# Performance work log

Hardware: AMD Instinct MI355X
Metric: run time of the kernel (lower is better)

Reference implementation:

```python
import jax, jax.numpy as jnp
import numpy as np

N_NODES = 10000
N_EDGES = 640000
D_IN = 128
D_OUT = 128


def setup_inputs() -> dict:
    key = jax.random.key(0)
    k1, k2, k3, k4 = jax.random.split(key, 4)
    x = jax.random.normal(k1, (N_NODES, D_IN), dtype=jnp.float32)
    # PyG GCNConv weight: [dim_out, dim_in] (glorot)
    W = jax.random.normal(k2, (D_OUT, D_IN), dtype=jnp.float32) * (1.0 / np.sqrt(D_IN))
    b = jnp.zeros((D_OUT,), dtype=jnp.float32)
    edge_weight = jax.random.uniform(k3, (N_EDGES,), dtype=jnp.float32)
    edge_index = jax.random.randint(k4, (2, N_EDGES), 0, N_NODES, dtype=jnp.int32)
    return {"x": x, "W": W, "b": b, "edge_weight": edge_weight, "edge_index": edge_index}


def reference(x, W, b, edge_weight, edge_index):
    N = x.shape[0]
    # --- add self loops (fill weight = 1.0), PyG default ---
    loops = jnp.arange(N, dtype=edge_index.dtype)
    src = jnp.concatenate([edge_index[0], loops])
    dst = jnp.concatenate([edge_index[1], loops])
    ew = jnp.concatenate([edge_weight, jnp.ones((N,), dtype=edge_weight.dtype)])
    # --- symmetric GCN normalization: deg from target index ---
    deg = jax.ops.segment_sum(ew, dst, num_segments=N)
    dinv = jnp.where(deg > 0, jax.lax.rsqrt(deg), 0.0)
    norm = dinv[src] * ew * dinv[dst]  # [E+N]
    # --- linear transform then gather-scale-scatter aggregation ---
    h = x @ W.T  # [N, D_OUT]
    msgs = h[src] * norm[:, None]  # [E+N, D_OUT]
    out = jax.ops.segment_sum(msgs, dst, num_segments=N)
    return out + b
```

## Files before the change

### kernel.cpp

```cpp
#include <hip/hip_runtime.h>

#define N_NODES 10000
#define N_EDGES 640000
#define D 128
#define CAP 128

typedef unsigned long long ull;
typedef unsigned short u16;
typedef unsigned int u32;

#define CHUNKS 256
#define EPC 2500
#define GEMM_NPB 32
#define GEMM_BLOCKS ((N_NODES + GEMM_NPB - 1) / GEMM_NPB)
#define SMEM_BYTES 40000
#define EWFX 262144.0f
#define EWM  0x1ffffffu

__device__ __forceinline__ u16 f2bf(float f) {
    unsigned u = __float_as_uint(f);
    unsigned r = (u + 0x7fffu + ((u >> 16) & 1u)) >> 16;
    return (u16)r;
}


__global__ void __launch_bounds__(256, 4) k_hist_fill_gemm(
    const int* __restrict__ src, const int* __restrict__ dst,
    const float* __restrict__ ew, u32* __restrict__ gpacked,
    const float* __restrict__ x, const float* __restrict__ W,
    u16* __restrict__ h_bf, ull* __restrict__ csr)
{
    extern __shared__ char smem[];
    const int t = threadIdx.x;

    if (blockIdx.x < CHUNKS) {
        u32* hist = (u32*)smem;
        ull* h8 = (ull*)smem;
        for (int i = t; i < N_NODES / 2; i += 256) h8[i] = 0;
        __syncthreads();

        const int e0 = blockIdx.x * EPC;
        u32 dlr[10];
        float ewr[10];
        #pragma unroll
        for (int i = 0; i < 10; ++i) {
            int idx = i * 256 + t;
            dlr[i] = 0xffffffffu;
            if (idx < EPC) {
                int e = e0 + idx;
                int d = dst[e];
                float w = ew[e];
                ewr[i] = w;
                u32 add = (1u << 25) | (u32)(w * EWFX);
                u32 old = atomicAdd(&hist[d], add);
                dlr[i] = ((u32)d << 7) | (old >> 25);
            }
        }
        __syncthreads();

        const int off = blockIdx.x * (N_NODES / CHUNKS);
        for (int ii = t; ii < N_NODES; ii += 256) {
            int i = ii + off;
            if (i >= N_NODES) i -= N_NODES;
            u32 v = hist[i];
            if (v) {
                u32 old = atomicAdd(&gpacked[i], v);
                hist[i] = old >> 25;
            }
        }
        __syncthreads();

        #pragma unroll
        for (int i = 0; i < 10; ++i) {
            if (dlr[i] != 0xffffffffu) {
                int e = e0 + i * 256 + t;
                int d = (int)(dlr[i] >> 7);
                int lr = (int)(dlr[i] & 127u);
                int slot = (int)hist[d] + lr;
                csr[(size_t)d * CAP + slot] =
                    ((ull)__float_as_uint(ewr[i]) << 32) | (unsigned)src[e];
            }
        }
    } else {
        float* xs = (float*)smem;
        const int gb = blockIdx.x - CHUNKS;
        const int node0 = gb * GEMM_NPB;
        const int col = t & 127;
        const int half = t >> 7;

        #pragma unroll
        for (int r = 0; r < 16; ++r) {
            int row = half * 16 + r;
            int n = node0 + row;
            xs[row * D + col] = (n < N_NODES) ? x[n * D + col] : 0.0f;
        }
        __syncthreads();

        float acc[16];
        #pragma unroll
        for (int r = 0; r < 16; ++r) acc[r] = 0.0f;

        const float4* Wrow = (const float4*)&W[col * D];
        const float* xbase = &xs[half * 16 * D];
        for (int k4 = 0; k4 < D / 4; ++k4) {
            float4 w = Wrow[k4];
            int k = k4 * 4;
            #pragma unroll
            for (int r = 0; r < 16; ++r) {
                acc[r] += xbase[r * D + k + 0] * w.x;
                acc[r] += xbase[r * D + k + 1] * w.y;
                acc[r] += xbase[r * D + k + 2] * w.z;
                acc[r] += xbase[r * D + k + 3] * w.w;
            }
        }
        #pragma unroll
        for (int r = 0; r < 16; ++r) {
            int n = node0 + half * 16 + r;
            if (n < N_NODES) h_bf[n * D + col] = f2bf(acc[r]);
        }
    }
}


#define AGG_NPB 4

__global__ void __launch_bounds__(256) k_agg(
    const u32* __restrict__ gpacked, const ull* __restrict__ csr,
    const u16* __restrict__ h_bf, const float* __restrict__ b,
    float* __restrict__ out)
{
    const int wid  = threadIdx.x >> 6;
    const int lane = threadIdx.x & 63;
    const int n = blockIdx.x * AGG_NPB + wid;

    __shared__ ull sm[AGG_NPB][CAP];

    const u32 gp = gpacked[n];
    const int deg = (int)(gp >> 25);
    const float dn = rsqrtf(1.0f + (float)(gp & EWM) * 0x1p-18f);
    const ull* bucket = csr + (size_t)n * CAP;

    #pragma unroll
    for (int r = 0; r < 2; ++r) {
        int j = r * 64 + lane;
        if (j < deg) {
            ull v = bucket[j];
            int s = (int)(u32)(v & 0xffffffffu);
            float w = __uint_as_float((u32)(v >> 32));
            u32 gs = gpacked[s];
            float ds_ = rsqrtf(1.0f + (float)(gs & EWM) * 0x1p-18f);
            float nm = ds_ * w * dn;
            sm[wid][j] = ((ull)__float_as_uint(nm) << 32) | (u32)s;
        }
    }
    __syncthreads();

    float acc0 = 0.0f, acc1 = 0.0f;
    const ull* smw = sm[wid];
    #pragma unroll 4
    for (int j = 0; j < deg; ++j) {
        ull v = smw[j];
        int s = (int)(u32)v;
        float nm = __uint_as_float((u32)(v >> 32));
        u32 hc = *(const u32*)(h_bf + (size_t)s * D + lane * 2);
        acc0 += __uint_as_float(hc << 16) * nm;
        acc1 += __uint_as_float(hc & 0xffff0000u) * nm;
    }

    float s2 = dn * dn;
    u32 hs = *(const u32*)(h_bf + (size_t)n * D + lane * 2);
    acc0 += __uint_as_float(hs << 16) * s2;
    acc1 += __uint_as_float(hs & 0xffff0000u) * s2;
    float2 bb = *(const float2*)(b + lane * 2);
    float2 o;
    o.x = acc0 + bb.x;
    o.y = acc1 + bb.y;
    *(float2*)(out + (size_t)n * D + lane * 2) = o;
}


extern "C" void kernel_launch(void* const* d_in, const int* in_sizes, int n_in,
                              void* d_out, int out_size, void* d_ws, size_t ws_size,
                              hipStream_t stream) {
    const float* x  = (const float*)d_in[0];
    const float* W  = (const float*)d_in[1];
    const float* b  = (const float*)d_in[2];
    const float* ew = (const float*)d_in[3];
    const int* ei   = (const int*)d_in[4];
    const int* src = ei;
    const int* dst = ei + N_EDGES;
    float* out = (float*)d_out;

    char* ws = (char*)d_ws;
    u32*   gpacked = (u32*)(ws);
    u16*   h_bf    = (u16*)(ws + 40000);
    ull*   csr     = (ull*)(ws + 2600000);

    hipMemsetAsync(gpacked, 0, 40000, stream);
    k_hist_fill_gemm<<<CHUNKS + GEMM_BLOCKS, 256, SMEM_BYTES, stream>>>(
        src, dst, ew, gpacked, x, W, h_bf, csr);
    k_agg<<<N_NODES / AGG_NPB, 256, 0, stream>>>(gpacked, csr, h_bf, b, out);
}
```

Before: 117.0 us.

## Replace shared-memory histogram CSR build with direct global atomics per edge

Drops the per-chunk shared-memory histogram, the merge into global counters and the two-pass slot assignment. Each thread now loads 4 edges with vector loads and does a global atomicAdd on the packed degree/weight counter, using the returned count directly as the CSR slot. GEMM blocks are placed first in the grid and use static shared memory. This removes two block-wide barriers and the sweep over the 10000-entry histogram, but increases global atomic traffic to one atomic per edge, with contention on hot destinations.

```diff
diff --git a/kernel.cpp b/kernel.cpp
--- a/kernel.cpp
+++ b/kernel.cpp
@@ -9,11 +9,11 @@
 typedef unsigned short u16;
 typedef unsigned int u32;
 
-#define CHUNKS 256
-#define EPC 2500
 #define GEMM_NPB 32
 #define GEMM_BLOCKS ((N_NODES + GEMM_NPB - 1) / GEMM_NPB)
-#define SMEM_BYTES 40000
+#define EPT 4
+#define EPB (256 * EPT)
+#define EDGE_BLOCKS (N_EDGES / EPB)
 #define EWFX 262144.0f
 #define EWM  0x1ffffffu
 
@@ -24,67 +24,33 @@
 }
 
 
-__global__ void __launch_bounds__(256, 4) k_hist_fill_gemm(
+__global__ void __launch_bounds__(256) k_build(
     const int* __restrict__ src, const int* __restrict__ dst,
     const float* __restrict__ ew, u32* __restrict__ gpacked,
     const float* __restrict__ x, const float* __restrict__ W,
     u16* __restrict__ h_bf, ull* __restrict__ csr)
 {
-    extern __shared__ char smem[];
+    __shared__ float xs[GEMM_NPB * D];
     const int t = threadIdx.x;
 
-    if (blockIdx.x < CHUNKS) {
-        u32* hist = (u32*)smem;
-        ull* h8 = (ull*)smem;
-        for (int i = t; i < N_NODES / 2; i += 256) h8[i] = 0;
-        __syncthreads();
-
-        const int e0 = blockIdx.x * EPC;
-        u32 dlr[10];
-        float ewr[10];
+    if (blockIdx.x >= GEMM_BLOCKS) {
+        const int e0 = (blockIdx.x - GEMM_BLOCKS) * EPB + t * EPT;
+        int4   dd = *(const int4*)(dst + e0);
+        int4   ss = *(const int4*)(src + e0);
+        float4 ww = *(const float4*)(ew + e0);
+        int   d_[4] = { dd.x, dd.y, dd.z, dd.w };
+        int   s_[4] = { ss.x, ss.y, ss.z, ss.w };
+        float w_[4] = { ww.x, ww.y, ww.z, ww.w };
         #pragma unroll
-        for (int i = 0; i < 10; ++i) {
-            int idx = i * 256 + t;
-            dlr[i] = 0xffffffffu;
-            if (idx < EPC) {
-                int e = e0 + idx;
-                int d = dst[e];
-                float w = ew[e];
-                ewr[i] = w;
-                u32 add = (1u << 25) | (u32)(w * EWFX);
-                u32 old = atomicAdd(&hist[d], add);
-                dlr[i] = ((u32)d << 7) | (old >> 25);
-            }
-        }
-        __syncthreads();
-
-        const int off = blockIdx.x * (N_NODES / CHUNKS);
-        for (int ii = t; ii < N_NODES; ii += 256) {
-            int i = ii + off;
-            if (i >= N_NODES) i -= N_NODES;
-            u32 v = hist[i];
-            if (v) {
-                u32 old = atomicAdd(&gpacked[i], v);
-                hist[i] = old >> 25;
-            }
-        }
-        __syncthreads();
-
-        #pragma unroll
-        for (int i = 0; i < 10; ++i) {
-            if (dlr[i] != 0xffffffffu) {
-                int e = e0 + i * 256 + t;
-                int d = (int)(dlr[i] >> 7);
-                int lr = (int)(dlr[i] & 127u);
-                int slot = (int)hist[d] + lr;
-                csr[(size_t)d * CAP + slot] =
-                    ((ull)__float_as_uint(ewr[i]) << 32) | (unsigned)src[e];
-            }
+        for (int i = 0; i < 4; ++i) {
+            u32 add = (1u << 25) | (u32)(w_[i] * EWFX);
+            u32 old = atomicAdd(&gpacked[d_[i]], add);
+            int slot = (int)(old >> 25);
+            csr[(size_t)d_[i] * CAP + slot] =
+                ((ull)__float_as_uint(w_[i]) << 32) | (u32)s_[i];
         }
     } else {
-        float* xs = (float*)smem;
-        const int gb = blockIdx.x - CHUNKS;
-        const int node0 = gb * GEMM_NPB;
+        const int node0 = blockIdx.x * GEMM_NPB;
         const int col = t & 127;
         const int half = t >> 7;
 
@@ -197,7 +163,7 @@
     ull*   csr     = (ull*)(ws + 2600000);
 
     hipMemsetAsync(gpacked, 0, 40000, stream);
-    k_hist_fill_gemm<<<CHUNKS + GEMM_BLOCKS, 256, SMEM_BYTES, stream>>>(
+    k_build<<<GEMM_BLOCKS + EDGE_BLOCKS, 256, 0, stream>>>(
         src, dst, ew, gpacked, x, W, h_bf, csr);
     k_agg<<<N_NODES / AGG_NPB, 256, 0, stream>>>(gpacked, csr, h_bf, b, out);
 }
```

After: 142.1 us. +21.5%, slower.
